# Optimization experiments

Measured on AMD Instinct MI355X. Metric: run time of the kernel, lower is better.

Reference implementation:

```python
import jax, jax.numpy as jnp
import numpy as np

DIM = 1024
KEY = 128
UV = 1024  # dim * mlp_ratio // 2
SCALE = 1.0 / np.sqrt(KEY).astype(np.float32)
NEG_INF = 1e12


def _sinusoidal(n, d):
    # RoPE tables: sin/cos of shape [n, d//2]
    pos = np.arange(n)[:, None].astype(np.float32)
    inv = (1.0 / 10000 ** (np.arange(0, d, 2).astype(np.float32) / d))[None, :]
    ang = pos * inv
    return jnp.asarray(np.sin(ang)), jnp.asarray(np.cos(ang))


def setup_inputs() -> dict:
    key = jax.random.key(0)
    ks = jax.random.split(key, 4)
    B, N = 4, 2048
    hidden_states = jax.random.normal(ks[0], (B, N, DIM), dtype=jnp.float32)
    attention_mask = jax.random.randint(ks[1], (B, N, N), 0, 2).astype(jnp.int32)
    sin, cos = _sinusoidal(N, KEY)
    Wi = jax.random.normal(ks[2], (DIM, UV * 2 + KEY), dtype=jnp.float32) * (DIM ** -0.5)
    bi = jnp.zeros((UV * 2 + KEY,), jnp.float32)
    Wo = jax.random.normal(ks[3], (UV, DIM), dtype=jnp.float32) * (UV ** -0.5)
    bo = jnp.zeros((DIM,), jnp.float32)
    return {
        "hidden_states": hidden_states, "attention_mask": attention_mask,
        "sin": sin, "cos": cos, "Wi": Wi, "bi": bi, "Wo": Wo, "bo": bo,
        "q_gamma": jnp.ones((KEY,), jnp.float32), "q_beta": jnp.zeros((KEY,), jnp.float32),
        "k_gamma": jnp.ones((KEY,), jnp.float32), "k_beta": jnp.zeros((KEY,), jnp.float32),
    }


def _rotary(x, sin, cos):
    # x: [b, n, d]; sin/cos: [n, d//2]; interleaved RoPE, concat layout
    x1, x2 = x[..., 0::2], x[..., 1::2]
    return jnp.concatenate([x1 * cos - x2 * sin, x1 * sin + x2 * cos], axis=-1)


def reference(hidden_states, attention_mask, sin, cos, Wi, bi, Wo, bo,
              q_gamma, q_beta, k_gamma, k_beta):
    x = jax.nn.silu(hidden_states @ Wi + bi)            # [b, n, 2176]
    u, v, qk = x[..., :UV], x[..., UV:2 * UV], x[..., 2 * UV:]
    q = _rotary(qk * q_gamma + q_beta, sin, cos)        # [b, n, 128]
    k = _rotary(qk * k_gamma + k_beta, sin, cos)
    a = jnp.einsum('bmd,bnd->bmn', q, k) * SCALE        # [b, m, n]
    mask = attention_mask != 0
    a = jnp.where(mask, a, -NEG_INF)
    ll = attention_mask.sum(-1, keepdims=True).astype(a.dtype)  # [b, m, 1]
    A = jnp.square(jax.nn.relu(a)) / ll                 # squared_relu normalize
    out = (u * jnp.einsum('bmn,bnd->bmd', A, v)) @ Wo + bo
    return out
```

## Files before the change

kernel.cpp:

```cpp
#include <hip/hip_runtime.h>
#include <hip/hip_bf16.h>
#include <cstdint>

#define DIM   1024
#define KEY   128
#define UV    1024
#define NCOL  (UV*2 + KEY)
#define SEQ   2048
#define BATCH 4
#define MTOT  (BATCH*SEQ)
#define SCALE 0.08838834764831845f

typedef __attribute__((ext_vector_type(8))) short short8;
typedef __attribute__((ext_vector_type(4))) float f32x4;

__device__ inline unsigned short f2b(float x) {
  unsigned int u = __float_as_uint(x);
  unsigned int r = (u + 0x7fffu + ((u >> 16) & 1u)) >> 16;
  return (unsigned short)r;
}
__device__ inline float b2f(unsigned short x) {
  return __uint_as_float(((unsigned int)x) << 16);
}

__device__ inline void gload_lds16(const void* g, void* l) {
  __builtin_amdgcn_global_load_lds(
      (const __attribute__((address_space(1))) unsigned int*)g,
      (__attribute__((address_space(3))) unsigned int*)l, 16, 0, 0);
}

__device__ __forceinline__ void gemm128(
    const unsigned short* __restrict__ A, int lda,
    const unsigned short* __restrict__ Bt, int ldb,
    int K, f32x4 acc[4][4], unsigned short* lds) {
  const int tid  = threadIdx.x;
  const int lane = tid & 63;
  const int wid  = tid >> 6;
  const int wr   = wid >> 1, wc = wid & 1;
  const int fr   = lane & 15;
  const int fq   = lane >> 4;

#pragma unroll
  for (int i = 0; i < 4; ++i)
#pragma unroll
    for (int j = 0; j < 4; ++j) acc[i][j] = (f32x4){0.f, 0.f, 0.f, 0.f};

  auto stage = [&](int k, int d) {
    unsigned short* la = lds + d * 8192;
    unsigned short* lb = la + 4096;
#pragma unroll
    for (int p = 0; p < 2; ++p) {
      int c = p * 256 + tid;
      int r = c >> 2, q = c & 3;
      int qs = q ^ ((r >> 1) & 3);
      gload_lds16(A + (size_t)r * lda + k * 32 + qs * 8,
                  la + (size_t)(p * 256 + wid * 64) * 8);
    }
#pragma unroll
    for (int p = 0; p < 2; ++p) {
      int c = p * 256 + tid;
      int r = c >> 2, q = c & 3;
      int qs = q ^ ((r >> 1) & 3);
      gload_lds16(Bt + (size_t)r * ldb + k * 32 + qs * 8,
                  lb + (size_t)(p * 256 + wid * 64) * 8);
    }
  };

  const int slot = (fq ^ ((fr >> 1) & 3)) * 8;
  const int rA   = (wr * 64 + fr) * 32 + slot;
  const int rB   = (wc * 64 + fr) * 32 + slot;

  const int NK = K >> 5;
  stage(0, 0);
  for (int k = 0; k < NK; ++k) {
    const int d = k & 1;
    if (k + 1 < NK) {
      stage(k + 1, d ^ 1);
      asm volatile("s_waitcnt vmcnt(4)" ::: "memory");
    } else {
      asm volatile("s_waitcnt vmcnt(0)" ::: "memory");
    }
    __builtin_amdgcn_s_barrier();
    asm volatile("" ::: "memory");
    const unsigned short* la = lds + d * 8192;
    const unsigned short* lb = la + 4096;
    short8 af[4], bf[4];
#pragma unroll
    for (int s = 0; s < 4; ++s) {
      af[s] = *(const short8*)&la[rA + s * 512];
      bf[s] = *(const short8*)&lb[rB + s * 512];
    }
#pragma unroll
    for (int i = 0; i < 4; ++i)
#pragma unroll
      for (int j = 0; j < 4; ++j)
        acc[i][j] = __builtin_amdgcn_mfma_f32_16x16x32_bf16(af[i], bf[j], acc[i][j], 0, 0, 0);
    asm volatile("" ::: "memory");
    __builtin_amdgcn_s_barrier();
    asm volatile("" ::: "memory");
  }
}

#define EPILOGUE_COORDS()                      \
  const int lane = threadIdx.x & 63;           \
  const int wid  = threadIdx.x >> 6;           \
  const int wr   = wid >> 1, wc = wid & 1;     \
  const int fr   = lane & 15;                  \
  const int fq   = lane >> 4;

__device__ __forceinline__ void xcd_swz(int& tx, int& ty) {
  const int gx = gridDim.x, gy = gridDim.y;
  const int n = gx * gy;
  const int D = blockIdx.y * gx + blockIdx.x;
  const int c = (D & 7) * (n >> 3) + (D >> 3);
  tx = c / gy;
  ty = c - tx * gy;
}

#define PREP_CVT   8192
#define PREP_MASK  2048
#define PREP_TWI   2176
#define PREP_TWO   1024

__global__ __launch_bounds__(256) void k_prep(
    const float* __restrict__ h, unsigned short* __restrict__ hbf,
    const int* __restrict__ mask, float* __restrict__ ll, unsigned int* __restrict__ mb,
    const float* __restrict__ Wi, unsigned short* __restrict__ WiT,
    const float* __restrict__ Wo, unsigned short* __restrict__ WoT) {
  __shared__ float t[32][33];
  const int bid = blockIdx.x;
  const int tid = threadIdx.x;

  if (bid < PREP_CVT) {
    int id = bid * 256 + tid;
    float4 f = ((const float4*)h)[id];
    ushort4 o;
    o.x = f2b(f.x); o.y = f2b(f.y); o.z = f2b(f.z); o.w = f2b(f.w);
    ((ushort4*)hbf)[id] = o;
  } else if (bid < PREP_CVT + PREP_MASK) {
    int wid = tid >> 6, lane = tid & 63;
    int row = (bid - PREP_CVT) * 4 + wid;
    const int4* p = (const int4*)(mask + (size_t)row * SEQ);
    int s = 0;
#pragma unroll
    for (int i = 0; i < 8; ++i) {
      int4 v = p[i * 64 + lane];
      unsigned nib = (v.x != 0 ? 1u : 0u) | (v.y != 0 ? 2u : 0u) |
                     (v.z != 0 ? 4u : 0u) | (v.w != 0 ? 8u : 0u);
      unsigned w = 0;
#pragma unroll
      for (int k2 = 0; k2 < 8; ++k2)
        w |= __shfl(nib, (lane & ~7) + k2, 64) << (4 * k2);
      if ((lane & 7) == 0) mb[(size_t)row * 64 + i * 8 + (lane >> 3)] = w;
      s += v.x + v.y + v.z + v.w;
    }
    for (int off = 32; off; off >>= 1) s += __shfl_down(s, off);
    if (lane == 0) ll[row] = (float)s;
  } else {
    const float* in; unsigned short* outp; int R, C, bx, by;
    if (bid < PREP_CVT + PREP_MASK + PREP_TWI) {
      int b = bid - (PREP_CVT + PREP_MASK);
      in = Wi; outp = WiT; R = DIM; C = NCOL; bx = b % 68; by = b / 68;
    } else {
      int b = bid - (PREP_CVT + PREP_MASK + PREP_TWI);
      in = Wo; outp = WoT; R = DIM; C = UV; bx = b & 31; by = b >> 5;
    }
    int c0 = bx * 32, r0 = by * 32;
    int tx = tid & 31, ty = tid >> 5;
#pragma unroll
    for (int i = 0; i < 4; ++i)
      t[ty + i * 8][tx] = in[(size_t)(r0 + ty + i * 8) * C + c0 + tx];
    __syncthreads();
#pragma unroll
    for (int i = 0; i < 4; ++i)
      outp[(size_t)(c0 + ty + i * 8) * R + r0 + tx] = f2b(t[tx][ty + i * 8]);
  }
}

__global__ __launch_bounds__(256, 4) void k_gemm1(const unsigned short* __restrict__ hbf,
                                                  const unsigned short* __restrict__ WiT,
                                                  const float* __restrict__ bi,
                                                  const float* __restrict__ sn,
                                                  const float* __restrict__ cs,
                                                  const float* __restrict__ qg,
                                                  const float* __restrict__ qb,
                                                  const float* __restrict__ kg,
                                                  const float* __restrict__ kb,
                                                  unsigned short* __restrict__ u,
                                                  unsigned short* __restrict__ vT,
                                                  unsigned short* __restrict__ qbuf,
                                                  unsigned short* __restrict__ kbuf) {
  __shared__ unsigned short lds[17408];
  int tx, ty; xcd_swz(tx, ty);
  int m0 = tx * 128, n0 = ty * 128;
  f32x4 acc[4][4];
  gemm128(hbf + (size_t)m0 * DIM, DIM, WiT + (size_t)n0 * DIM, DIM, DIM, acc, lds);
  EPILOGUE_COORDS();
  if (n0 < UV) {
#pragma unroll
    for (int i = 0; i < 4; ++i)
#pragma unroll
      for (int j = 0; j < 4; ++j)
#pragma unroll
        for (int r = 0; r < 4; ++r) {
          int row = m0 + wr * 64 + i * 16 + fq * 4 + r;
          int col = n0 + wc * 64 + j * 16 + fr;
          float x = acc[i][j][r] + bi[col];
          float s = x / (1.f + __expf(-x));
          u[(size_t)row * UV + col] = f2b(s);
        }
  } else if (n0 < 2 * UV) {
    unsigned short (*t)[136] = (unsigned short (*)[136])lds;
#pragma unroll
    for (int i = 0; i < 4; ++i)
#pragma unroll
      for (int j = 0; j < 4; ++j)
#pragma unroll
        for (int r = 0; r < 4; r += 2) {
          int rl = wr * 64 + i * 16 + fq * 4 + r;
          int dl = wc * 64 + j * 16 + fr;
          int col = n0 + dl;
          float x0 = acc[i][j][r]     + bi[col];
          float x1 = acc[i][j][r + 1] + bi[col];
          float s0 = x0 / (1.f + __expf(-x0));
          float s1 = x1 / (1.f + __expf(-x1));
          unsigned pk = (unsigned)f2b(s0) | ((unsigned)f2b(s1) << 16);
          *(unsigned*)&t[dl][rl] = pk;
        }
    __syncthreads();
    int bb = m0 >> 11;
    int ns = m0 & (SEQ - 1);
    int d0 = n0 - UV;
    const int tid = threadIdx.x;
#pragma unroll
    for (int it = 0; it < 8; ++it) {
      int idx = it * 256 + tid;
      int dl = idx >> 4, q = idx & 15;
      *(int4*)&vT[((size_t)bb * UV + d0 + dl) * SEQ + ns + q * 8] =
          *(const int4*)&t[dl][q * 8];
    }
  } else {
    const int colk_base = wc * 64;
    const bool ev = (fr & 1) == 0;
#pragma unroll
    for (int i = 0; i < 4; ++i)
#pragma unroll
      for (int j = 0; j < 4; ++j)
#pragma unroll
        for (int r = 0; r < 4; ++r) {
          int row  = m0 + wr * 64 + i * 16 + fq * 4 + r;
          int colk = colk_base + j * 16 + fr;
          float x = acc[i][j][r] + bi[2 * UV + colk];
          float s = x / (1.f + __expf(-x));
          float aq = s * qg[colk] + qb[colk];
          float ak = s * kg[colk] + kb[colk];
          float aqx = __shfl_xor(aq, 1);
          float akx = __shfl_xor(ak, 1);
          int t_ = colk >> 1;
          int n  = row & (SEQ - 1);
          float cc = cs[n * 64 + t_], ss = sn[n * 64 + t_];
          float q1 = ev ? aq : aqx, q2 = ev ? aqx : aq;
          float k1 = ev ? ak : akx, k2 = ev ? akx : ak;
          float resq = ev ? (q1 * cc - q2 * ss) : (q1 * ss + q2 * cc);
          float resk = ev ? (k1 * cc - k2 * ss) : (k1 * ss + k2 * cc);
          int oc = ev ? t_ : (64 + t_);
          qbuf[(size_t)row * KEY + oc] = f2b(resq);
          kbuf[(size_t)row * KEY + oc] = f2b(resk);
        }
  }
}

__global__ __launch_bounds__(256, 4) void k_qk(const unsigned short* __restrict__ q,
                                               const unsigned short* __restrict__ k,
                                               const unsigned int* __restrict__ mb,
                                               const float* __restrict__ ll,
                                               unsigned short* __restrict__ Abuf) {
  __shared__ unsigned short lds[16384];
  int b = blockIdx.z;
  int m0 = blockIdx.x * 128, n0 = blockIdx.y * 128;
  f32x4 acc[4][4];
  gemm128(q + ((size_t)b * SEQ + m0) * KEY, KEY,
          k + ((size_t)b * SEQ + n0) * KEY, KEY, KEY, acc, lds);
  EPILOGUE_COORDS();
#pragma unroll
  for (int i = 0; i < 4; ++i)
#pragma unroll
    for (int r = 0; r < 4; ++r) {
      int row = m0 + wr * 64 + i * 16 + fq * 4 + r;
      size_t rb = (size_t)b * SEQ + row;
      unsigned long long mw =
          *(const unsigned long long*)&mb[rb * 64 + (n0 >> 5) + wc * 2];
      float rll = 1.0f / ll[rb];
#pragma unroll
      for (int j = 0; j < 4; ++j) {
        int col = n0 + wc * 64 + j * 16 + fr;
        float a = acc[i][j][r] * SCALE;
        bool on = (mw >> (j * 16 + fr)) & 1ull;
        float rel = (on && a > 0.f) ? a : 0.f;
        Abuf[rb * SEQ + col] = f2b(rel * rel * rll);
      }
    }
}

__global__ __launch_bounds__(256, 4) void k_av(const unsigned short* __restrict__ Abuf,
                                               const unsigned short* __restrict__ vT,
                                               const unsigned short* __restrict__ u,
                                               unsigned short* __restrict__ g) {
  __shared__ unsigned short lds[16384];
  int b = blockIdx.z;
  int m0 = blockIdx.x * 128, n0 = blockIdx.y * 128;
  f32x4 acc[4][4];
  gemm128(Abuf + ((size_t)b * SEQ + m0) * SEQ, SEQ,
          vT + ((size_t)b * UV + n0) * SEQ, SEQ, SEQ, acc, lds);
  EPILOGUE_COORDS();
#pragma unroll
  for (int i = 0; i < 4; ++i)
#pragma unroll
    for (int j = 0; j < 4; ++j)
#pragma unroll
      for (int r = 0; r < 4; ++r) {
        int row = m0 + wr * 64 + i * 16 + fq * 4 + r;
        int col = n0 + wc * 64 + j * 16 + fr;
        size_t gi = ((size_t)b * SEQ + row) * UV + col;
        g[gi] = f2b(acc[i][j][r] * b2f(u[gi]));
      }
}

__global__ __launch_bounds__(256, 4) void k_out(const unsigned short* __restrict__ g,
                                                const unsigned short* __restrict__ WoT,
                                                const float* __restrict__ bo,
                                                float* __restrict__ out) {
  __shared__ unsigned short lds[16384];
  int m0 = blockIdx.x * 128, n0 = blockIdx.y * 128;
  f32x4 acc[4][4];
  gemm128(g + (size_t)m0 * UV, UV, WoT + (size_t)n0 * UV, UV, UV, acc, lds);
  EPILOGUE_COORDS();
#pragma unroll
  for (int i = 0; i < 4; ++i)
#pragma unroll
    for (int j = 0; j < 4; ++j)
#pragma unroll
      for (int r = 0; r < 4; ++r) {
        int row = m0 + wr * 64 + i * 16 + fq * 4 + r;
        int col = n0 + wc * 64 + j * 16 + fr;
        out[(size_t)row * DIM + col] = acc[i][j][r] + bo[col];
      }
}

extern "C" void kernel_launch(void* const* d_in, const int* in_sizes, int n_in,
                              void* d_out, int out_size, void* d_ws, size_t ws_size,
                              hipStream_t stream) {
  const float* h    = (const float*)d_in[0];
  const int*   mask = (const int*)d_in[1];
  const float* sn   = (const float*)d_in[2];
  const float* cs   = (const float*)d_in[3];
  const float* Wi   = (const float*)d_in[4];
  const float* bi   = (const float*)d_in[5];
  const float* Wo   = (const float*)d_in[6];
  const float* bo   = (const float*)d_in[7];
  const float* qg   = (const float*)d_in[8];
  const float* qb   = (const float*)d_in[9];
  const float* kg   = (const float*)d_in[10];
  const float* kb   = (const float*)d_in[11];
  float* out = (float*)d_out;

  char* ws = (char*)d_ws;
  size_t off = 0;
  auto alloc = [&](size_t bytes) { void* p = ws + off; off += (bytes + 255) & ~(size_t)255; return p; };
  unsigned short* hbf  = (unsigned short*)alloc((size_t)MTOT * DIM * 2);
  unsigned short* WiT  = (unsigned short*)alloc((size_t)NCOL * DIM * 2);
  unsigned short* WoT  = (unsigned short*)alloc((size_t)DIM * UV * 2);
  unsigned short* u    = (unsigned short*)alloc((size_t)MTOT * UV * 2);
  unsigned short* vT   = (unsigned short*)alloc((size_t)MTOT * UV * 2);
  unsigned short* qbuf = (unsigned short*)alloc((size_t)MTOT * KEY * 2);
  unsigned short* kbuf = (unsigned short*)alloc((size_t)MTOT * KEY * 2);
  float*          ll   = (float*)alloc((size_t)MTOT * 4);
  unsigned int*   mbits= (unsigned int*)alloc((size_t)MTOT * 64 * 4);
  unsigned short* Abuf = (unsigned short*)alloc((size_t)BATCH * SEQ * SEQ * 2);
  unsigned short* g    = (unsigned short*)alloc((size_t)MTOT * UV * 2);

  k_prep<<<PREP_CVT + PREP_MASK + PREP_TWI + PREP_TWO, 256, 0, stream>>>(
      h, hbf, mask, ll, mbits, Wi, WiT, Wo, WoT);

  k_gemm1<<<dim3(MTOT / 128, NCOL / 128), 256, 0, stream>>>(
      hbf, WiT, bi, sn, cs, qg, qb, kg, kb, u, vT, qbuf, kbuf);
  k_qk<<<dim3(SEQ / 128, SEQ / 128, BATCH), 256, 0, stream>>>(qbuf, kbuf, mbits, ll, Abuf);
  k_av<<<dim3(SEQ / 128, UV / 128, BATCH), 256, 0, stream>>>(Abuf, vT, u, g);
  k_out<<<dim3(MTOT / 128, DIM / 128), 256, 0, stream>>>(g, WoT, bo, out);
}
```

Baseline: 180.7 us.

## Split qk projection into split-K GEMM with separate rotary finalize kernel

The qk column tile of the first projection GEMM is moved out into its own kernel that splits the K dimension into four slices, writing fp32 partial sums. A new elementwise kernel reduces the partials and applies bias, SiLU, gamma/beta and RoPE. The goal is to shorten the tail caused by the single slow epilogue column of tiles and give that tile more parallelism. In exchange it adds two launches and roughly 16MB of fp32 partial traffic. The u/v GEMM grid shrinks to 16 column tiles.

```diff
diff --git a/kernel.cpp b/kernel.cpp
--- a/kernel.cpp
+++ b/kernel.cpp
@@ -177,19 +177,11 @@
   }
 }
 
-__global__ __launch_bounds__(256, 4) void k_gemm1(const unsigned short* __restrict__ hbf,
-                                                  const unsigned short* __restrict__ WiT,
-                                                  const float* __restrict__ bi,
-                                                  const float* __restrict__ sn,
-                                                  const float* __restrict__ cs,
-                                                  const float* __restrict__ qg,
-                                                  const float* __restrict__ qb,
-                                                  const float* __restrict__ kg,
-                                                  const float* __restrict__ kb,
-                                                  unsigned short* __restrict__ u,
-                                                  unsigned short* __restrict__ vT,
-                                                  unsigned short* __restrict__ qbuf,
-                                                  unsigned short* __restrict__ kbuf) {
+__global__ __launch_bounds__(256, 4) void k_gemm1a(const unsigned short* __restrict__ hbf,
+                                                   const unsigned short* __restrict__ WiT,
+                                                   const float* __restrict__ bi,
+                                                   unsigned short* __restrict__ u,
+                                                   unsigned short* __restrict__ vT) {
   __shared__ unsigned short lds[17408];
   int tx, ty; xcd_swz(tx, ty);
   int m0 = tx * 128, n0 = ty * 128;
@@ -209,7 +201,7 @@
           float s = x / (1.f + __expf(-x));
           u[(size_t)row * UV + col] = f2b(s);
         }
-  } else if (n0 < 2 * UV) {
+  } else {
     unsigned short (*t)[136] = (unsigned short (*)[136])lds;
 #pragma unroll
     for (int i = 0; i < 4; ++i)
@@ -239,35 +231,63 @@
       *(int4*)&vT[((size_t)bb * UV + d0 + dl) * SEQ + ns + q * 8] =
           *(const int4*)&t[dl][q * 8];
     }
-  } else {
-    const int colk_base = wc * 64;
-    const bool ev = (fr & 1) == 0;
-#pragma unroll
-    for (int i = 0; i < 4; ++i)
-#pragma unroll
-      for (int j = 0; j < 4; ++j)
-#pragma unroll
-        for (int r = 0; r < 4; ++r) {
-          int row  = m0 + wr * 64 + i * 16 + fq * 4 + r;
-          int colk = colk_base + j * 16 + fr;
-          float x = acc[i][j][r] + bi[2 * UV + colk];
-          float s = x / (1.f + __expf(-x));
-          float aq = s * qg[colk] + qb[colk];
-          float ak = s * kg[colk] + kb[colk];
-          float aqx = __shfl_xor(aq, 1);
-          float akx = __shfl_xor(ak, 1);
-          int t_ = colk >> 1;
-          int n  = row & (SEQ - 1);
-          float cc = cs[n * 64 + t_], ss = sn[n * 64 + t_];
-          float q1 = ev ? aq : aqx, q2 = ev ? aqx : aq;
-          float k1 = ev ? ak : akx, k2 = ev ? akx : ak;
-          float resq = ev ? (q1 * cc - q2 * ss) : (q1 * ss + q2 * cc);
-          float resk = ev ? (k1 * cc - k2 * ss) : (k1 * ss + k2 * cc);
-          int oc = ev ? t_ : (64 + t_);
-          qbuf[(size_t)row * KEY + oc] = f2b(resq);
-          kbuf[(size_t)row * KEY + oc] = f2b(resk);
-        }
   }
+}
+
+__global__ __launch_bounds__(256, 4) void k_gemm1b(const unsigned short* __restrict__ hbf,
+                                                   const unsigned short* __restrict__ WiT,
+                                                   float* __restrict__ qkp) {
+  __shared__ unsigned short lds[16384];
+  int m0 = blockIdx.x * 128;
+  int sl = blockIdx.y;
+  f32x4 acc[4][4];
+  gemm128(hbf + (size_t)m0 * DIM + sl * 256, DIM,
+          WiT + (size_t)(2 * UV) * DIM + sl * 256, DIM, 256, acc, lds);
+  EPILOGUE_COORDS();
+  float* dst = qkp + (size_t)sl * MTOT * KEY;
+#pragma unroll
+  for (int i = 0; i < 4; ++i)
+#pragma unroll
+    for (int j = 0; j < 4; ++j)
+#pragma unroll
+      for (int r = 0; r < 4; ++r) {
+        int row = m0 + wr * 64 + i * 16 + fq * 4 + r;
+        int col = wc * 64 + j * 16 + fr;
+        dst[(size_t)row * KEY + col] = acc[i][j][r];
+      }
+}
+
+__global__ __launch_bounds__(256) void k_rfin(const float* __restrict__ qkp,
+                                              const float* __restrict__ bi,
+                                              const float* __restrict__ sn,
+                                              const float* __restrict__ cs,
+                                              const float* __restrict__ qg,
+                                              const float* __restrict__ qb,
+                                              const float* __restrict__ kg,
+                                              const float* __restrict__ kb,
+                                              unsigned short* __restrict__ q,
+                                              unsigned short* __restrict__ k) {
+  int id = blockIdx.x * 256 + threadIdx.x;
+  int m = id >> 6, t = id & 63;
+  int n = m & (SEQ - 1);
+  const float2* p = (const float2*)qkp;
+  float2 s0 = p[(size_t)0 * MTOT * 64 + m * 64 + t];
+  float2 s1 = p[(size_t)1 * MTOT * 64 + m * 64 + t];
+  float2 s2 = p[(size_t)2 * MTOT * 64 + m * 64 + t];
+  float2 s3 = p[(size_t)3 * MTOT * 64 + m * 64 + t];
+  float x1 = s0.x + s1.x + s2.x + s3.x + bi[2 * UV + 2 * t];
+  float x2 = s0.y + s1.y + s2.y + s3.y + bi[2 * UV + 2 * t + 1];
+  float sa = x1 / (1.f + __expf(-x1));
+  float sb = x2 / (1.f + __expf(-x2));
+  float s_ = sn[n * 64 + t], c_ = cs[n * 64 + t];
+  float a1 = sa * qg[2 * t] + qb[2 * t];
+  float a2 = sb * qg[2 * t + 1] + qb[2 * t + 1];
+  q[m * KEY + t]      = f2b(a1 * c_ - a2 * s_);
+  q[m * KEY + 64 + t] = f2b(a1 * s_ + a2 * c_);
+  float b1 = sa * kg[2 * t] + kb[2 * t];
+  float b2 = sb * kg[2 * t + 1] + kb[2 * t + 1];
+  k[m * KEY + t]      = f2b(b1 * c_ - b2 * s_);
+  k[m * KEY + 64 + t] = f2b(b1 * s_ + b2 * c_);
 }
 
 __global__ __launch_bounds__(256, 4) void k_qk(const unsigned short* __restrict__ q,
@@ -374,6 +394,7 @@
   unsigned short* vT   = (unsigned short*)alloc((size_t)MTOT * UV * 2);
   unsigned short* qbuf = (unsigned short*)alloc((size_t)MTOT * KEY * 2);
   unsigned short* kbuf = (unsigned short*)alloc((size_t)MTOT * KEY * 2);
+  float*          qkp  = (float*)alloc((size_t)4 * MTOT * KEY * 4);
   float*          ll   = (float*)alloc((size_t)MTOT * 4);
   unsigned int*   mbits= (unsigned int*)alloc((size_t)MTOT * 64 * 4);
   unsigned short* Abuf = (unsigned short*)alloc((size_t)BATCH * SEQ * SEQ * 2);
@@ -382,8 +403,9 @@
   k_prep<<<PREP_CVT + PREP_MASK + PREP_TWI + PREP_TWO, 256, 0, stream>>>(
       h, hbf, mask, ll, mbits, Wi, WiT, Wo, WoT);
 
-  k_gemm1<<<dim3(MTOT / 128, NCOL / 128), 256, 0, stream>>>(
-      hbf, WiT, bi, sn, cs, qg, qb, kg, kb, u, vT, qbuf, kbuf);
+  k_gemm1b<<<dim3(MTOT / 128, 4), 256, 0, stream>>>(hbf, WiT, qkp);
+  k_gemm1a<<<dim3(MTOT / 128, 16), 256, 0, stream>>>(hbf, WiT, bi, u, vT);
+  k_rfin<<<(MTOT * 64) / 256, 256, 0, stream>>>(qkp, bi, sn, cs, qg, qb, kg, kb, qbuf, kbuf);
   k_qk<<<dim3(SEQ / 128, SEQ / 128, BATCH), 256, 0, stream>>>(qbuf, kbuf, mbits, ll, Abuf);
   k_av<<<dim3(SEQ / 128, UV / 128, BATCH), 256, 0, stream>>>(Abuf, vT, u, g);
   k_out<<<dim3(MTOT / 128, DIM / 128), 256, 0, stream>>>(g, WoT, bo, out);
```

New measurement: 172.7 us, median of 2. 1.05x faster.
